# Kernel optimization log

Hardware: AMD Instinct MI355X
Metric: run time of the kernel (lower is better)

The kernel has to match this reference:

```python
import jax, jax.numpy as jnp
import numpy as np

N_NODES = 50000
N_EDGES = 800000
N_GRAPHS = 64
IN_DIM = 128
HID = 32
HEADS = 4
EDGE_DIM = 8
OUT = 10


def setup_inputs() -> dict:
    key = jax.random.key(0)
    ks = jax.random.split(key, 20)
    s = 0.1
    inp = {
        "x": jax.random.normal(ks[0], (N_NODES, IN_DIM), jnp.float32),
        "edge_index": jax.random.randint(ks[1], (2, N_EDGES), 0, N_NODES, jnp.int32),
        "edge_attr": jax.random.normal(ks[2], (N_EDGES, EDGE_DIM), jnp.float32),
        "batch": jnp.sort(jax.random.randint(ks[3], (N_NODES,), 0, N_GRAPHS, jnp.int32)),
        # conv1: heads=4, out=32
        "W1": jax.random.normal(ks[4], (IN_DIM, HEADS * HID), jnp.float32) * s,
        "att_src1": jax.random.normal(ks[5], (HEADS, HID), jnp.float32) * s,
        "att_dst1": jax.random.normal(ks[6], (HEADS, HID), jnp.float32) * s,
        "We1": jax.random.normal(ks[7], (EDGE_DIM, HEADS * HID), jnp.float32) * s,
        "att_e1": jax.random.normal(ks[8], (HEADS, HID), jnp.float32) * s,
        "b1": jnp.zeros((HEADS * HID,), jnp.float32),
        # conv2: heads=1, out=32
        "W2": jax.random.normal(ks[9], (HEADS * HID, HID), jnp.float32) * s,
        "att_src2": jax.random.normal(ks[10], (1, HID), jnp.float32) * s,
        "att_dst2": jax.random.normal(ks[11], (1, HID), jnp.float32) * s,
        "We2": jax.random.normal(ks[12], (EDGE_DIM, HID), jnp.float32) * s,
        "att_e2": jax.random.normal(ks[13], (1, HID), jnp.float32) * s,
        "b2": jnp.zeros((HID,), jnp.float32),
        # MLP head
        "W3": jax.random.normal(ks[14], (HID, HID // 2), jnp.float32) * s,
        "b3": jnp.zeros((HID // 2,), jnp.float32),
        "W4": jax.random.normal(ks[15], (HID // 2, OUT), jnp.float32) * s,
        "b4": jnp.zeros((OUT,), jnp.float32),
    }
    return inp


def _gat_conv(x, src, dst, eattr, W, a_s, a_d, We, a_e, b, H, C, N):
    """PyG GATConv math (self-loops already appended to src/dst/eattr)."""
    h = (x @ W).reshape(-1, H, C)            # [N,H,C]
    e = (eattr @ We).reshape(-1, H, C)       # [E,H,C]
    al_s = jnp.sum(h * a_s, -1)              # [N,H]
    al_d = jnp.sum(h * a_d, -1)              # [N,H]
    alpha = al_s[src] + al_d[dst] + jnp.sum(e * a_e, -1)   # [E,H]
    alpha = jax.nn.leaky_relu(alpha, 0.2)
    # segment softmax over incoming edges of each dst node
    m = jax.ops.segment_max(alpha, dst, num_segments=N)
    ealpha = jnp.exp(alpha - m[dst])
    denom = jax.ops.segment_sum(ealpha, dst, num_segments=N)
    ealpha = ealpha / (denom[dst] + 1e-16)
    msg = h[src] * ealpha[:, :, None]        # [E,H,C]
    out = jax.ops.segment_sum(msg, dst, num_segments=N)  # [N,H,C]
    return out.reshape(N, H * C) + b


def _forward(x, edge_index, edge_attr, batch,
             W1, att_src1, att_dst1, We1, att_e1, b1,
             W2, att_src2, att_dst2, We2, att_e2, b2,
             W3, b3, W4, b4):
    N = x.shape[0]
    src, dst = edge_index[0], edge_index[1]
    # add_self_loops with fill_value='mean': loop attr = mean of incoming edge_attr
    cnt = jax.ops.segment_sum(jnp.ones((src.shape[0],), x.dtype), dst, num_segments=N)
    loop_attr = jax.ops.segment_sum(edge_attr, dst, num_segments=N) / jnp.maximum(cnt, 1.0)[:, None]
    ar = jnp.arange(N, dtype=src.dtype)
    src2 = jnp.concatenate([src, ar])
    dst2 = jnp.concatenate([dst, ar])
    eattr2 = jnp.concatenate([edge_attr, loop_attr], axis=0)

    h = _gat_conv(x, src2, dst2, eattr2, W1, att_src1, att_dst1, We1, att_e1, b1, HEADS, HID, N)
    h = jax.nn.elu(h)
    h = _gat_conv(h, src2, dst2, eattr2, W2, att_src2, att_dst2, We2, att_e2, b2, 1, HID, N)
    h = jax.nn.elu(h)
    # global mean pool per graph
    gsum = jax.ops.segment_sum(h, batch, num_segments=N_GRAPHS)
    gcnt = jax.ops.segment_sum(jnp.ones((N,), h.dtype), batch, num_segments=N_GRAPHS)
    g = gsum / jnp.maximum(gcnt, 1.0)[:, None]
    # MLP head (eval mode: dropout is identity)
    z = jax.nn.relu(g @ W3 + b3)
    return z @ W4 + b4


def reference(x, edge_index, edge_attr, batch,
              W1, att_src1, att_dst1, We1, att_e1, b1,
              W2, att_src2, att_dst2, We2, att_e2, b2,
              W3, b3, W4, b4):
    return _forward(x, edge_index, edge_attr, batch,
                    W1, att_src1, att_dst1, We1, att_e1, b1,
                    W2, att_src2, att_dst2, We2, att_e2, b2,
                    W3, b3, W4, b4)
```

## Files before the change

kernel.cpp:

```cpp
#include <hip/hip_runtime.h>
#include <hip/hip_bf16.h>
#include <math.h>

#define N_NODES 50000
#define N_EDGES 800000
#define N_GRAPHS 64
#define IN_DIM 128
#define HID 32
#define HEADS 4
#define EDGE_DIM 8
#define OUT_DIM 10
#define HC 128
#define NB 196
#define EBLK 3125
#define G1HALF 391

__device__ __forceinline__ float leaky(float x){ return x >= 0.f ? x : 0.2f*x; }
__device__ __forceinline__ float elu_f(float x){ return x > 0.f ? x : __expf(x)-1.f; }

__device__ __forceinline__ float bf2f(unsigned short u){
  union { unsigned int i; float f; } v; v.i = ((unsigned int)u) << 16; return v.f;
}
__device__ __forceinline__ unsigned short f2bf(float f){
  union { float f; unsigned int i; } v; v.f = f;
  unsigned int r = v.i + 0x7FFF + ((v.i >> 16) & 1);
  return (unsigned short)(r >> 16);
}

__device__ __forceinline__ void gemm1_body(int bb, float* xs, float* ws,
    const float* __restrict__ x, const float* __restrict__ W1,
    const float* __restrict__ as1, const float* __restrict__ ad1,
    unsigned short* __restrict__ h1b, float* __restrict__ als1, float* __restrict__ ald1){
  int t = threadIdx.x;
  int cg = t & 15, c8 = cg*8, qb = (t >> 4)*4;
  int base = bb * 64;
  for (int i = t; i < 2048; i += 256){
    int node = base + (i >> 5);
    int col = (i & 31) * 4;
    float4 v = make_float4(0,0,0,0);
    if (node < N_NODES) v = *(const float4*)&x[node*IN_DIM + col];
    *(float4*)&xs[(i>>5)*128 + col] = v;
  }
  float acc[4][8];
  #pragma unroll
  for (int q = 0; q < 4; q++)
    #pragma unroll
    for (int i = 0; i < 8; i++) acc[q][i] = 0.f;

  for (int kb = 0; kb < 128; kb += 64){
    __syncthreads();
    for (int i = t; i < 2048; i += 256)
      *(float4*)&ws[i*4] = *(const float4*)&W1[kb*128 + i*4];
    __syncthreads();
    #pragma unroll 4
    for (int k = 0; k < 64; k++){
      float4 w0 = *(float4*)&ws[k*128 + c8];
      float4 w1 = *(float4*)&ws[k*128 + c8 + 4];
      #pragma unroll
      for (int q = 0; q < 4; q++){
        float xv = xs[(qb + q)*128 + kb + k];
        acc[q][0] = fmaf(xv, w0.x, acc[q][0]);
        acc[q][1] = fmaf(xv, w0.y, acc[q][1]);
        acc[q][2] = fmaf(xv, w0.z, acc[q][2]);
        acc[q][3] = fmaf(xv, w0.w, acc[q][3]);
        acc[q][4] = fmaf(xv, w1.x, acc[q][4]);
        acc[q][5] = fmaf(xv, w1.y, acc[q][5]);
        acc[q][6] = fmaf(xv, w1.z, acc[q][6]);
        acc[q][7] = fmaf(xv, w1.w, acc[q][7]);
      }
    }
  }
  int head = cg >> 2;
  float asv[8], adv[8];
  #pragma unroll
  for (int i = 0; i < 8; i++){ asv[i] = as1[c8 + i]; adv[i] = ad1[c8 + i]; }
  #pragma unroll
  for (int q = 0; q < 4; q++){
    int n = base + qb + q;
    if (n >= N_NODES) continue;
    float sa = 0.f, sd = 0.f;
    #pragma unroll
    for (int i = 0; i < 8; i++){
      sa = fmaf(acc[q][i], asv[i], sa);
      sd = fmaf(acc[q][i], adv[i], sd);
    }
    sa += __shfl_xor(sa, 1); sd += __shfl_xor(sd, 1);
    sa += __shfl_xor(sa, 2); sd += __shfl_xor(sd, 2);
    uint4 pk;
    pk.x = (unsigned int)f2bf(acc[q][0]) | ((unsigned int)f2bf(acc[q][1]) << 16);
    pk.y = (unsigned int)f2bf(acc[q][2]) | ((unsigned int)f2bf(acc[q][3]) << 16);
    pk.z = (unsigned int)f2bf(acc[q][4]) | ((unsigned int)f2bf(acc[q][5]) << 16);
    pk.w = (unsigned int)f2bf(acc[q][6]) | ((unsigned int)f2bf(acc[q][7]) << 16);
    *(uint4*)&h1b[n*HC + c8] = pk;
    if ((cg & 3) == 0){ als1[n*4 + head] = sa; ald1[n*4 + head] = sd; }
  }
}

__global__ __launch_bounds__(256) void k_f1(const int* __restrict__ dst, int* __restrict__ cnt,
    const float* __restrict__ x, const float* __restrict__ W1,
    const float* __restrict__ as1, const float* __restrict__ ad1,
    unsigned short* __restrict__ h1b, float* __restrict__ als1, float* __restrict__ ald1){
  __shared__ float smem[16384];
  int m = blockIdx.x % 9, r = blockIdx.x / 9;
  if (m < 8){
    int e = (r*8 + m)*256 + threadIdx.x;
    if (e < N_EDGES) atomicAdd(&cnt[dst[e]], 1);
    return;
  }
  gemm1_body(r, smem, smem + 8192, x, W1, as1, ad1, h1b, als1, ald1);
}

__global__ __launch_bounds__(256) void k_blocksum(const int* __restrict__ cnt, int* __restrict__ bsum){
  __shared__ int sh[256];
  int n = blockIdx.x*256 + threadIdx.x;
  sh[threadIdx.x] = (n < N_NODES) ? cnt[n] : 0;
  __syncthreads();
  for (int off = 128; off > 0; off >>= 1){
    if (threadIdx.x < off) sh[threadIdx.x] += sh[threadIdx.x + off];
    __syncthreads();
  }
  if (threadIdx.x == 0) bsum[blockIdx.x] = sh[0];
}

__global__ __launch_bounds__(256) void k_scanb(const int* __restrict__ bsum, int* __restrict__ bpre){
  __shared__ int sh[256];
  int t = threadIdx.x;
  int v = (t < NB) ? bsum[t] : 0;
  sh[t] = v; __syncthreads();
  for (int off = 1; off < 256; off <<= 1){
    int u = (t >= off) ? sh[t-off] : 0;
    __syncthreads();
    sh[t] += u;
    __syncthreads();
  }
  if (t < NB) bpre[t] = sh[t] - v;
}

__global__ __launch_bounds__(256) void k_rowptr(const int* __restrict__ cnt, const int* __restrict__ bpre,
    int* __restrict__ rowptr, int* __restrict__ wofs){
  __shared__ int sh[256];
  int t = threadIdx.x; int n = blockIdx.x*256 + t;
  int c = (n < N_NODES) ? cnt[n] : 0;
  sh[t] = c; __syncthreads();
  for (int off = 1; off < 256; off <<= 1){
    int u = (t >= off) ? sh[t-off] : 0;
    __syncthreads();
    sh[t] += u;
    __syncthreads();
  }
  int incl = sh[t];
  if (n < N_NODES){
    int rp = bpre[blockIdx.x] + incl - c;
    rowptr[n] = rp;
    wofs[n] = rp;
  }
  if (n == N_NODES-1) rowptr[N_NODES] = bpre[blockIdx.x] + incl;
}

__global__ __launch_bounds__(256) void k_f2(const int* __restrict__ src, const int* __restrict__ dst,
    const float* __restrict__ eattr,
    const float* __restrict__ We1, const float* __restrict__ ae1w,
    const float* __restrict__ We2, const float* __restrict__ ae2w,
    int* __restrict__ wofs, int4* __restrict__ rec,
    const float* __restrict__ x, const float* __restrict__ W1,
    const float* __restrict__ as1, const float* __restrict__ ad1,
    unsigned short* __restrict__ h1b, float* __restrict__ als1, float* __restrict__ ald1){
  __shared__ float smem[16384];
  int m = blockIdx.x % 9, r = blockIdx.x / 9;
  if (m < 8){
    int t = threadIdx.x;
    if (t < 32){
      int d = t >> 2, h = t & 3;
      float s = 0.f;
      for (int c = 0; c < 32; c++) s = fmaf(We1[d*128 + h*32 + c], ae1w[h*32 + c], s);
      smem[d*4 + h] = s;
    } else if (t < 40){
      int d = t - 32;
      float s = 0.f;
      for (int c = 0; c < 32; c++) s = fmaf(We2[d*32 + c], ae2w[c], s);
      smem[32 + d] = s;
    }
    __syncthreads();
    int e = (r*8 + m)*256 + t;
    if (e >= N_EDGES) return;
    int sv = src[e], d = dst[e];
    float4 x0 = *(const float4*)&eattr[e*8];
    float4 x1 = *(const float4*)&eattr[e*8+4];
    float ea[8] = {x0.x,x0.y,x0.z,x0.w,x1.x,x1.y,x1.z,x1.w};
    float4 rr = make_float4(0,0,0,0);
    float r2 = 0.f;
    #pragma unroll
    for (int dd = 0; dd < 8; dd++){
      rr.x = fmaf(ea[dd], smem[dd*4+0], rr.x);
      rr.y = fmaf(ea[dd], smem[dd*4+1], rr.y);
      rr.z = fmaf(ea[dd], smem[dd*4+2], rr.z);
      rr.w = fmaf(ea[dd], smem[dd*4+3], rr.w);
      r2   = fmaf(ea[dd], smem[32+dd], r2);
    }
    int pos = atomicAdd(&wofs[d], 1);
    int4 rv;
    rv.x = sv;
    rv.y = (int)((unsigned int)f2bf(rr.x) | ((unsigned int)f2bf(rr.y) << 16));
    rv.z = (int)((unsigned int)f2bf(rr.z) | ((unsigned int)f2bf(rr.w) << 16));
    rv.w = __float_as_int(r2);
    rec[pos] = rv;
    return;
  }
  gemm1_body(G1HALF + r, smem, smem + 8192, x, W1, as1, ad1, h1b, als1, ald1);
}

__global__ __launch_bounds__(256) void k_conv1(const int* __restrict__ rowptr, const int4* __restrict__ rec,
    const float* __restrict__ als1, const float* __restrict__ ald1,
    const unsigned short* __restrict__ h1b, const float* __restrict__ b1,
    unsigned short* __restrict__ heb){
  int wv = threadIdx.x >> 6, l = threadIdx.x & 63;
  int n = blockIdx.x*4 + wv;
  if (n >= N_NODES) return;
  int c0 = l*2, h = l >> 4;
  int hs1 = (h & 1) * 16;
  float ad = ald1[n*4 + h];
  float den = 0.f, sum_ae = 0.f;
  float2 acc = make_float2(0.f, 0.f);
  int r0 = rowptr[n], r1 = rowptr[n+1];
  int k = r0;
  for (; k + 2 <= r1; k += 2){
    int4 q0 = rec[k], q1 = rec[k+1];
    unsigned int w0 = (h & 2) ? (unsigned int)q0.z : (unsigned int)q0.y;
    unsigned int w1 = (h & 2) ? (unsigned int)q1.z : (unsigned int)q1.y;
    float ae_0 = bf2f((unsigned short)(w0 >> hs1));
    float ae_1 = bf2f((unsigned short)(w1 >> hs1));
    float as_0 = als1[q0.x*4 + h], as_1 = als1[q1.x*4 + h];
    unsigned int hv0 = *(const unsigned int*)(h1b + q0.x*HC + c0);
    unsigned int hv1 = *(const unsigned int*)(h1b + q1.x*HC + c0);
    float p0 = __expf(leaky(as_0 + ad + ae_0));
    float p1 = __expf(leaky(as_1 + ad + ae_1));
    sum_ae += ae_0 + ae_1;
    den += p0 + p1;
    acc.x = fmaf(p0, bf2f((unsigned short)hv0), acc.x);
    acc.y = fmaf(p0, bf2f((unsigned short)(hv0 >> 16)), acc.y);
    acc.x = fmaf(p1, bf2f((unsigned short)hv1), acc.x);
    acc.y = fmaf(p1, bf2f((unsigned short)(hv1 >> 16)), acc.y);
  }
  if (k < r1){
    int4 q = rec[k];
    unsigned int w = (h & 2) ? (unsigned int)q.z : (unsigned int)q.y;
    float aev = bf2f((unsigned short)(w >> hs1));
    float p = __expf(leaky(als1[q.x*4 + h] + ad + aev));
    unsigned int hv = *(const unsigned int*)(h1b + q.x*HC + c0);
    sum_ae += aev; den += p;
    acc.x = fmaf(p, bf2f((unsigned short)hv), acc.x);
    acc.y = fmaf(p, bf2f((unsigned short)(hv >> 16)), acc.y);
  }
  int cn = r1 - r0; if (cn < 1) cn = 1;
  float ps = __expf(leaky(als1[n*4 + h] + ad + sum_ae / (float)cn));
  unsigned int hs = *(const unsigned int*)(h1b + n*HC + c0);
  den += ps;
  acc.x = fmaf(ps, bf2f((unsigned short)hs), acc.x);
  acc.y = fmaf(ps, bf2f((unsigned short)(hs >> 16)), acc.y);
  float inv = 1.f / (den + 1e-16f);
  float o0 = elu_f(fmaf(acc.x, inv, b1[c0]));
  float o1 = elu_f(fmaf(acc.y, inv, b1[c0+1]));
  *(unsigned int*)(heb + n*HC + c0) =
      (unsigned int)f2bf(o0) | ((unsigned int)f2bf(o1) << 16);
}

__global__ __launch_bounds__(256) void k_gemm2(const unsigned short* __restrict__ heb,
    const float* __restrict__ W2, const float* __restrict__ as2, const float* __restrict__ ad2,
    unsigned short* __restrict__ h2b, float* __restrict__ als2, float* __restrict__ ald2){
  __shared__ float ws[128*32];
  __shared__ float xs[16][128];
  int t = threadIdx.x; int c = t & 31; int j = t >> 5;
  int base = blockIdx.x * 16;
  for (int i = t; i < 1024; i += 256)
    *(float4*)&ws[i*4] = *(const float4*)&W2[i*4];
  {
    int node = base + (t >> 4);
    int col = (t & 15) * 8;
    uint4 v = make_uint4(0,0,0,0);
    if (node < N_NODES) v = *(const uint4*)(heb + node*128 + col);
    float* xp = &xs[t>>4][col];
    xp[0] = bf2f((unsigned short)v.x); xp[1] = bf2f((unsigned short)(v.x>>16));
    xp[2] = bf2f((unsigned short)v.y); xp[3] = bf2f((unsigned short)(v.y>>16));
    xp[4] = bf2f((unsigned short)v.z); xp[5] = bf2f((unsigned short)(v.z>>16));
    xp[6] = bf2f((unsigned short)v.w); xp[7] = bf2f((unsigned short)(v.w>>16));
  }
  __syncthreads();
  float s0 = 0.f, s1 = 0.f;
  #pragma unroll 8
  for (int k = 0; k < 128; k++){
    float w = ws[k*32 + c];
    s0 = fmaf(xs[j*2][k],   w, s0);
    s1 = fmaf(xs[j*2+1][k], w, s1);
  }
  float a2c = as2[c], d2c = ad2[c];
  int n0 = base + j*2, n1 = n0 + 1;
  float sa0 = s0*a2c, sd0 = s0*d2c, sa1 = s1*a2c, sd1 = s1*d2c;
  #pragma unroll
  for (int off = 1; off < 32; off <<= 1){
    sa0 += __shfl_xor(sa0, off); sd0 += __shfl_xor(sd0, off);
    sa1 += __shfl_xor(sa1, off); sd1 += __shfl_xor(sd1, off);
  }
  if (n0 < N_NODES){ h2b[n0*32 + c] = f2bf(s0); if (c == 0){ als2[n0] = sa0; ald2[n0] = sd0; } }
  if (n1 < N_NODES){ h2b[n1*32 + c] = f2bf(s1); if (c == 0){ als2[n1] = sa1; ald2[n1] = sd1; } }
}

__global__ __launch_bounds__(256) void k_conv2(const int* __restrict__ rowptr, const int4* __restrict__ rec,
    const float* __restrict__ als2, const float* __restrict__ ald2,
    const unsigned short* __restrict__ h2b, const float* __restrict__ b2, float* __restrict__ out2){
  int wv = threadIdx.x >> 6, l = threadIdx.x & 63;
  int n = blockIdx.x*4 + wv;
  if (n >= N_NODES) return;
  int half = l >> 5, c = l & 31;
  float ad = ald2[n];
  int r0 = rowptr[n], r1 = rowptr[n+1];
  int h0 = (r1 - r0 + 1) >> 1;
  int ks = half ? r0 + h0 : r0;
  int ke = half ? r1 : r0 + h0;
  float den = 0.f, acc = 0.f, sum_ae = 0.f;
  int k = ks;
  for (; k + 2 <= ke; k += 2){
    int4 q0 = rec[k], q1 = rec[k+1];
    float ae_0 = __int_as_float(q0.w), ae_1 = __int_as_float(q1.w);
    float as_0 = als2[q0.x], as_1 = als2[q1.x];
    float hv0 = bf2f(h2b[q0.x*32 + c]);
    float hv1 = bf2f(h2b[q1.x*32 + c]);
    float p0 = __expf(leaky(as_0 + ad + ae_0));
    float p1 = __expf(leaky(as_1 + ad + ae_1));
    sum_ae += ae_0 + ae_1;
    den += p0 + p1;
    acc = fmaf(p0, hv0, acc);
    acc = fmaf(p1, hv1, acc);
  }
  if (k < ke){
    int4 q = rec[k];
    float aev = __int_as_float(q.w);
    float p = __expf(leaky(als2[q.x] + ad + aev));
    float hv = bf2f(h2b[q.x*32 + c]);
    sum_ae += aev; den += p;
    acc = fmaf(p, hv, acc);
  }
  den += __shfl_xor(den, 32);
  acc += __shfl_xor(acc, 32);
  sum_ae += __shfl_xor(sum_ae, 32);
  int cn = r1 - r0; if (cn < 1) cn = 1;
  float ps = __expf(leaky(als2[n] + ad + sum_ae / (float)cn));
  den += ps;
  acc = fmaf(ps, bf2f(h2b[n*32 + c]), acc);
  float val = acc / (den + 1e-16f) + b2[c];
  if (half == 0) out2[n*32 + c] = elu_f(val);
}

__global__ __launch_bounds__(256) void k_pool(const float* __restrict__ out2, const int* __restrict__ batch,
    float* __restrict__ gpool){
  int g = blockIdx.x;
  int a = 0, b = N_NODES;
  while (a < b){ int mid = (a + b) >> 1; if (batch[mid] < g) a = mid + 1; else b = mid; }
  int lo = a;
  a = lo; b = N_NODES;
  while (a < b){ int mid = (a + b) >> 1; if (batch[mid] < g + 1) a = mid + 1; else b = mid; }
  int hi = a;
  int t = threadIdx.x, c = t & 31, r = t >> 5;
  float s = 0.f;
  for (int n = lo + r; n < hi; n += 8) s += out2[n*32 + c];
  __shared__ float sh[256];
  sh[t] = s; __syncthreads();
  if (r == 0){
    for (int q = 1; q < 8; q++) s += sh[q*32 + c];
    int cg = hi - lo; if (cg < 1) cg = 1;
    gpool[g*32 + c] = s / (float)cg;
  }
}

__global__ __launch_bounds__(1024) void k_mlp(const float* __restrict__ gpool, const float* __restrict__ W3,
    const float* __restrict__ b3, const float* __restrict__ W4, const float* __restrict__ b4,
    float* __restrict__ out){
  __shared__ float z[64*16];
  int t = threadIdx.x;
  {
    int g = t >> 4, jj = t & 15;
    float s = b3[jj];
    #pragma unroll
    for (int c = 0; c < 32; c++) s = fmaf(gpool[g*32 + c], W3[c*16 + jj], s);
    z[t] = fmaxf(s, 0.f);
  }
  __syncthreads();
  if (t < 640){
    int g = t / 10, o = t - g*10;
    float s = b4[o];
    #pragma unroll
    for (int jj = 0; jj < 16; jj++) s = fmaf(z[g*16 + jj], W4[jj*10 + o], s);
    out[t] = s;
  }
}

extern "C" void kernel_launch(void* const* d_in, const int* in_sizes, int n_in,
                              void* d_out, int out_size, void* d_ws, size_t ws_size,
                              hipStream_t stream) {
  (void)in_sizes; (void)n_in; (void)out_size; (void)ws_size;
  const float* x     = (const float*)d_in[0];
  const int*   ei    = (const int*)  d_in[1];
  const float* eattr = (const float*)d_in[2];
  const int*   batch = (const int*)  d_in[3];
  const float* W1    = (const float*)d_in[4];
  const float* as1   = (const float*)d_in[5];
  const float* ad1   = (const float*)d_in[6];
  const float* We1   = (const float*)d_in[7];
  const float* ae1w  = (const float*)d_in[8];
  const float* b1    = (const float*)d_in[9];
  const float* W2    = (const float*)d_in[10];
  const float* as2   = (const float*)d_in[11];
  const float* ad2   = (const float*)d_in[12];
  const float* We2   = (const float*)d_in[13];
  const float* ae2w  = (const float*)d_in[14];
  const float* b2    = (const float*)d_in[15];
  const float* W3    = (const float*)d_in[16];
  const float* b3    = (const float*)d_in[17];
  const float* W4    = (const float*)d_in[18];
  const float* b4    = (const float*)d_in[19];
  float* out = (float*)d_out;
  const int* src  = ei;
  const int* dstp = ei + N_EDGES;

  char* p = (char*)d_ws;
  auto alloc = [&](size_t bytes)->void*{ void* r = (void*)p; p += (bytes + 255) & ~(size_t)255; return r; };
  int*    cnt      = (int*)   alloc(4*N_NODES);
  size_t  zero_bytes = (size_t)(p - (char*)d_ws);
  int*    wofs     = (int*)   alloc(4*N_NODES);
  int*    rowptr   = (int*)   alloc(4*(N_NODES+1));
  int*    bsum     = (int*)   alloc(4*NB);
  int*    bpre     = (int*)   alloc(4*NB);
  int4*   rec      = (int4*)  alloc(16*N_EDGES);
  unsigned short* h1b  = (unsigned short*)alloc(2*N_NODES*HC);
  float*  als1     = (float*) alloc(16*N_NODES);
  float*  ald1     = (float*) alloc(16*N_NODES);
  unsigned short* heb  = (unsigned short*)alloc(2*N_NODES*HC);
  unsigned short* h2b  = (unsigned short*)alloc(2*N_NODES*HID);
  float*  als2     = (float*) alloc(4*N_NODES);
  float*  ald2     = (float*) alloc(4*N_NODES);
  float*  out2     = (float*) alloc(4*N_NODES*HID);
  float*  gpool    = (float*) alloc(4*N_GRAPHS*HID);

  const int FGRID = G1HALF * 9;

  hipMemsetAsync(d_ws, 0, zero_bytes, stream);
  k_f1      <<<FGRID, 256, 0, stream>>>(dstp, cnt, x, W1, as1, ad1, h1b, als1, ald1);
  k_blocksum<<<NB,    256, 0, stream>>>(cnt, bsum);
  k_scanb   <<<1,     256, 0, stream>>>(bsum, bpre);
  k_rowptr  <<<NB,    256, 0, stream>>>(cnt, bpre, rowptr, wofs);
  k_f2      <<<FGRID, 256, 0, stream>>>(src, dstp, eattr, We1, ae1w, We2, ae2w,
                                        wofs, rec, x, W1, as1, ad1, h1b, als1, ald1);
  k_conv1   <<<(N_NODES+3)/4, 256, 0, stream>>>(rowptr, rec, als1, ald1, h1b, b1, heb);
  k_gemm2   <<<(N_NODES+15)/16, 256, 0, stream>>>(heb, W2, as2, ad2, h2b, als2, ald2);
  k_conv2   <<<(N_NODES+3)/4, 256, 0, stream>>>(rowptr, rec, als2, ald2, h2b, b2, out2);
  k_pool    <<<N_GRAPHS, 256, 0, stream>>>(out2, batch, gpool);
  k_mlp     <<<1,    1024, 0, stream>>>(gpool, W3, b3, W4, b4, out);
}
```

Measured before the change: 381.4 us.

## Precompute per-edge attention weights and self-loop terms before aggregation kernels

```diff
diff --git a/kernel.cpp b/kernel.cpp
--- a/kernel.cpp
+++ b/kernel.cpp
@@ -13,7 +13,7 @@
 #define HC 128
 #define NB 196
 #define EBLK 3125
-#define G1HALF 391
+#define G1BLK 782
 
 __device__ __forceinline__ float leaky(float x){ return x >= 0.f ? x : 0.2f*x; }
 __device__ __forceinline__ float elu_f(float x){ return x > 0.f ? x : __expf(x)-1.f; }
@@ -25,6 +25,9 @@
   union { float f; unsigned int i; } v; v.f = f;
   unsigned int r = v.i + 0x7FFF + ((v.i >> 16) & 1);
   return (unsigned short)(r >> 16);
+}
+__device__ __forceinline__ unsigned int pk2(float a, float b){
+  return (unsigned int)f2bf(a) | ((unsigned int)f2bf(b) << 16);
 }
 
 __device__ __forceinline__ void gemm1_body(int bb, float* xs, float* ws,
@@ -39,7 +42,7 @@
     int col = (i & 31) * 4;
     float4 v = make_float4(0,0,0,0);
     if (node < N_NODES) v = *(const float4*)&x[node*IN_DIM + col];
-    *(float4*)&xs[(i>>5)*128 + col] = v;
+    *(float4*)&xs[(i>>5)*132 + col] = v;
   }
   float acc[4][8];
   #pragma unroll
@@ -47,18 +50,21 @@
     #pragma unroll
     for (int i = 0; i < 8; i++) acc[q][i] = 0.f;
 
-  for (int kb = 0; kb < 128; kb += 64){
-    __syncthreads();
-    for (int i = t; i < 2048; i += 256)
-      *(float4*)&ws[i*4] = *(const float4*)&W1[kb*128 + i*4];
+  for (int kb = 0; kb < 128; kb += 32){
+    __syncthreads();
+    for (int i = t; i < 1024; i += 256){
+      int k = i >> 5, col4 = i & 31;
+      int pcg = col4 >> 1, plane = col4 & 1;
+      *(float4*)&ws[plane*2048 + k*64 + pcg*4] = *(const float4*)&W1[(kb+k)*128 + col4*4];
+    }
     __syncthreads();
     #pragma unroll 4
-    for (int k = 0; k < 64; k++){
-      float4 w0 = *(float4*)&ws[k*128 + c8];
-      float4 w1 = *(float4*)&ws[k*128 + c8 + 4];
+    for (int k = 0; k < 32; k++){
+      float4 w0 = *(float4*)&ws[k*64 + cg*4];
+      float4 w1 = *(float4*)&ws[2048 + k*64 + cg*4];
       #pragma unroll
       for (int q = 0; q < 4; q++){
-        float xv = xs[(qb + q)*128 + kb + k];
+        float xv = xs[(qb + q)*132 + kb + k];
         acc[q][0] = fmaf(xv, w0.x, acc[q][0]);
         acc[q][1] = fmaf(xv, w0.y, acc[q][1]);
         acc[q][2] = fmaf(xv, w0.z, acc[q][2]);
@@ -87,10 +93,10 @@
     sa += __shfl_xor(sa, 1); sd += __shfl_xor(sd, 1);
     sa += __shfl_xor(sa, 2); sd += __shfl_xor(sd, 2);
     uint4 pk;
-    pk.x = (unsigned int)f2bf(acc[q][0]) | ((unsigned int)f2bf(acc[q][1]) << 16);
-    pk.y = (unsigned int)f2bf(acc[q][2]) | ((unsigned int)f2bf(acc[q][3]) << 16);
-    pk.z = (unsigned int)f2bf(acc[q][4]) | ((unsigned int)f2bf(acc[q][5]) << 16);
-    pk.w = (unsigned int)f2bf(acc[q][6]) | ((unsigned int)f2bf(acc[q][7]) << 16);
+    pk.x = pk2(acc[q][0], acc[q][1]);
+    pk.y = pk2(acc[q][2], acc[q][3]);
+    pk.z = pk2(acc[q][4], acc[q][5]);
+    pk.w = pk2(acc[q][6], acc[q][7]);
     *(uint4*)&h1b[n*HC + c8] = pk;
     if ((cg & 3) == 0){ als1[n*4 + head] = sa; ald1[n*4 + head] = sd; }
   }
@@ -100,14 +106,14 @@
     const float* __restrict__ x, const float* __restrict__ W1,
     const float* __restrict__ as1, const float* __restrict__ ad1,
     unsigned short* __restrict__ h1b, float* __restrict__ als1, float* __restrict__ ald1){
-  __shared__ float smem[16384];
-  int m = blockIdx.x % 9, r = blockIdx.x / 9;
-  if (m < 8){
-    int e = (r*8 + m)*256 + threadIdx.x;
+  __shared__ float smem[12544];
+  int m = blockIdx.x % 5, r = blockIdx.x / 5;
+  if (m < 4){
+    int e = (r*4 + m)*256 + threadIdx.x;
     if (e < N_EDGES) atomicAdd(&cnt[dst[e]], 1);
     return;
   }
-  gemm1_body(r, smem, smem + 8192, x, W1, as1, ad1, h1b, als1, ald1);
+  gemm1_body(r, smem, smem + 8448, x, W1, as1, ad1, h1b, als1, ald1);
 }
 
 __global__ __launch_bounds__(256) void k_blocksum(const int* __restrict__ cnt, int* __restrict__ bsum){
@@ -157,84 +163,134 @@
   if (n == N_NODES-1) rowptr[N_NODES] = bpre[blockIdx.x] + incl;
 }
 
+__device__ __forceinline__ void v_smem(float* v,
+    const float* __restrict__ We1, const float* __restrict__ ae1w,
+    const float* __restrict__ We2, const float* __restrict__ ae2w){
+  int t = threadIdx.x;
+  if (t < 32){
+    int d = t >> 2, h = t & 3;
+    float s = 0.f;
+    for (int c = 0; c < 32; c++) s = fmaf(We1[d*128 + h*32 + c], ae1w[h*32 + c], s);
+    v[d*4 + h] = s;
+  } else if (t < 40){
+    int d = t - 32;
+    float s = 0.f;
+    for (int c = 0; c < 32; c++) s = fmaf(We2[d*32 + c], ae2w[c], s);
+    v[32 + d] = s;
+  }
+  __syncthreads();
+}
+
 __global__ __launch_bounds__(256) void k_f2(const int* __restrict__ src, const int* __restrict__ dst,
     const float* __restrict__ eattr,
     const float* __restrict__ We1, const float* __restrict__ ae1w,
     const float* __restrict__ We2, const float* __restrict__ ae2w,
-    int* __restrict__ wofs, int4* __restrict__ rec,
-    const float* __restrict__ x, const float* __restrict__ W1,
-    const float* __restrict__ as1, const float* __restrict__ ad1,
-    unsigned short* __restrict__ h1b, float* __restrict__ als1, float* __restrict__ ald1){
-  __shared__ float smem[16384];
-  int m = blockIdx.x % 9, r = blockIdx.x / 9;
-  if (m < 8){
-    int t = threadIdx.x;
-    if (t < 32){
-      int d = t >> 2, h = t & 3;
-      float s = 0.f;
-      for (int c = 0; c < 32; c++) s = fmaf(We1[d*128 + h*32 + c], ae1w[h*32 + c], s);
-      smem[d*4 + h] = s;
-    } else if (t < 40){
-      int d = t - 32;
-      float s = 0.f;
-      for (int c = 0; c < 32; c++) s = fmaf(We2[d*32 + c], ae2w[c], s);
-      smem[32 + d] = s;
-    }
-    __syncthreads();
-    int e = (r*8 + m)*256 + t;
-    if (e >= N_EDGES) return;
-    int sv = src[e], d = dst[e];
-    float4 x0 = *(const float4*)&eattr[e*8];
-    float4 x1 = *(const float4*)&eattr[e*8+4];
-    float ea[8] = {x0.x,x0.y,x0.z,x0.w,x1.x,x1.y,x1.z,x1.w};
-    float4 rr = make_float4(0,0,0,0);
-    float r2 = 0.f;
-    #pragma unroll
-    for (int dd = 0; dd < 8; dd++){
-      rr.x = fmaf(ea[dd], smem[dd*4+0], rr.x);
-      rr.y = fmaf(ea[dd], smem[dd*4+1], rr.y);
-      rr.z = fmaf(ea[dd], smem[dd*4+2], rr.z);
-      rr.w = fmaf(ea[dd], smem[dd*4+3], rr.w);
-      r2   = fmaf(ea[dd], smem[32+dd], r2);
-    }
-    int pos = atomicAdd(&wofs[d], 1);
-    int4 rv;
-    rv.x = sv;
-    rv.y = (int)((unsigned int)f2bf(rr.x) | ((unsigned int)f2bf(rr.y) << 16));
-    rv.z = (int)((unsigned int)f2bf(rr.z) | ((unsigned int)f2bf(rr.w) << 16));
-    rv.w = __float_as_int(r2);
-    rec[pos] = rv;
-    return;
-  }
-  gemm1_body(G1HALF + r, smem, smem + 8192, x, W1, as1, ad1, h1b, als1, ald1);
+    const float* __restrict__ als1, const float* __restrict__ ald1,
+    int* __restrict__ wofs, int4* __restrict__ rec, uint4* __restrict__ rec2){
+  __shared__ float v[40];
+  v_smem(v, We1, ae1w, We2, ae2w);
+  int e = blockIdx.x*256 + threadIdx.x;
+  if (e >= N_EDGES) return;
+  int sv = src[e], d = dst[e];
+  float4 x0 = *(const float4*)&eattr[e*8];
+  float4 x1 = *(const float4*)&eattr[e*8+4];
+  float ea[8] = {x0.x,x0.y,x0.z,x0.w,x1.x,x1.y,x1.z,x1.w};
+  float4 r = make_float4(0,0,0,0);
+  float r2 = 0.f;
+  #pragma unroll
+  for (int dd = 0; dd < 8; dd++){
+    r.x = fmaf(ea[dd], v[dd*4+0], r.x);
+    r.y = fmaf(ea[dd], v[dd*4+1], r.y);
+    r.z = fmaf(ea[dd], v[dd*4+2], r.z);
+    r.w = fmaf(ea[dd], v[dd*4+3], r.w);
+    r2  = fmaf(ea[dd], v[32+dd], r2);
+  }
+  float4 as = *(const float4*)&als1[sv*4];
+  float4 ad = *(const float4*)&ald1[d*4];
+  float p0 = __expf(leaky(as.x + ad.x + r.x));
+  float p1 = __expf(leaky(as.y + ad.y + r.y));
+  float p2 = __expf(leaky(as.z + ad.z + r.z));
+  float p3 = __expf(leaky(as.w + ad.w + r.w));
+  int pos = atomicAdd(&wofs[d], 1);
+  int4 rv;
+  rv.x = sv;
+  rv.y = (int)pk2(p0, p1);
+  rv.z = (int)pk2(p2, p3);
+  rv.w = __float_as_int(r2);
+  rec[pos] = rv;
+  uint4 e2;
+  e2.x = pk2(ea[0], ea[1]); e2.y = pk2(ea[2], ea[3]);
+  e2.z = pk2(ea[4], ea[5]); e2.w = pk2(ea[6], ea[7]);
+  rec2[pos] = e2;
+}
+
+__global__ __launch_bounds__(256) void k_self(const int* __restrict__ rowptr,
+    const uint4* __restrict__ rec2, const float* __restrict__ als1, const float* __restrict__ ald1,
+    const float* __restrict__ We1, const float* __restrict__ ae1w,
+    const float* __restrict__ We2, const float* __restrict__ ae2w,
+    float* __restrict__ pself1, float* __restrict__ mae2){
+  __shared__ float v[40];
+  v_smem(v, We1, ae1w, We2, ae2w);
+  int n = blockIdx.x*256 + threadIdx.x;
+  if (n >= N_NODES) return;
+  int r0 = rowptr[n], r1 = rowptr[n+1];
+  float s[8];
+  #pragma unroll
+  for (int i = 0; i < 8; i++) s[i] = 0.f;
+  for (int k = r0; k < r1; k++){
+    uint4 q = rec2[k];
+    s[0] += bf2f((unsigned short)q.x); s[1] += bf2f((unsigned short)(q.x >> 16));
+    s[2] += bf2f((unsigned short)q.y); s[3] += bf2f((unsigned short)(q.y >> 16));
+    s[4] += bf2f((unsigned short)q.z); s[5] += bf2f((unsigned short)(q.z >> 16));
+    s[6] += bf2f((unsigned short)q.w); s[7] += bf2f((unsigned short)(q.w >> 16));
+  }
+  int cn = r1 - r0; if (cn < 1) cn = 1;
+  float inv = 1.f / (float)cn;
+  float m1[4] = {0.f, 0.f, 0.f, 0.f};
+  float m2 = 0.f;
+  #pragma unroll
+  for (int dd = 0; dd < 8; dd++){
+    float mv = s[dd] * inv;
+    m1[0] = fmaf(mv, v[dd*4+0], m1[0]);
+    m1[1] = fmaf(mv, v[dd*4+1], m1[1]);
+    m1[2] = fmaf(mv, v[dd*4+2], m1[2]);
+    m1[3] = fmaf(mv, v[dd*4+3], m1[3]);
+    m2    = fmaf(mv, v[32+dd], m2);
+  }
+  float4 as = *(const float4*)&als1[n*4];
+  float4 ad = *(const float4*)&ald1[n*4];
+  float4 p;
+  p.x = __expf(leaky(as.x + ad.x + m1[0]));
+  p.y = __expf(leaky(as.y + ad.y + m1[1]));
+  p.z = __expf(leaky(as.z + ad.z + m1[2]));
+  p.w = __expf(leaky(as.w + ad.w + m1[3]));
+  *(float4*)&pself1[n*4] = p;
+  mae2[n] = m2;
 }
 
 __global__ __launch_bounds__(256) void k_conv1(const int* __restrict__ rowptr, const int4* __restrict__ rec,
-    const float* __restrict__ als1, const float* __restrict__ ald1,
-    const unsigned short* __restrict__ h1b, const float* __restrict__ b1,
-    unsigned short* __restrict__ heb){
+    const float* __restrict__ pself1, const unsigned short* __restrict__ h1b,
+    const float* __restrict__ b1, unsigned short* __restrict__ heb){
   int wv = threadIdx.x >> 6, l = threadIdx.x & 63;
   int n = blockIdx.x*4 + wv;
   if (n >= N_NODES) return;
   int c0 = l*2, h = l >> 4;
   int hs1 = (h & 1) * 16;
-  float ad = ald1[n*4 + h];
-  float den = 0.f, sum_ae = 0.f;
-  float2 acc = make_float2(0.f, 0.f);
+  float ps = pself1[n*4 + h];
+  unsigned int hsv = *(const unsigned int*)(h1b + n*HC + c0);
+  float den = ps;
+  float2 acc = make_float2(ps * bf2f((unsigned short)hsv),
+                           ps * bf2f((unsigned short)(hsv >> 16)));
   int r0 = rowptr[n], r1 = rowptr[n+1];
   int k = r0;
   for (; k + 2 <= r1; k += 2){
     int4 q0 = rec[k], q1 = rec[k+1];
     unsigned int w0 = (h & 2) ? (unsigned int)q0.z : (unsigned int)q0.y;
     unsigned int w1 = (h & 2) ? (unsigned int)q1.z : (unsigned int)q1.y;
-    float ae_0 = bf2f((unsigned short)(w0 >> hs1));
-    float ae_1 = bf2f((unsigned short)(w1 >> hs1));
-    float as_0 = als1[q0.x*4 + h], as_1 = als1[q1.x*4 + h];
+    float p0 = bf2f((unsigned short)(w0 >> hs1));
+    float p1 = bf2f((unsigned short)(w1 >> hs1));
     unsigned int hv0 = *(const unsigned int*)(h1b + q0.x*HC + c0);
     unsigned int hv1 = *(const unsigned int*)(h1b + q1.x*HC + c0);
-    float p0 = __expf(leaky(as_0 + ad + ae_0));
-    float p1 = __expf(leaky(as_1 + ad + ae_1));
-    sum_ae += ae_0 + ae_1;
     den += p0 + p1;
     acc.x = fmaf(p0, bf2f((unsigned short)hv0), acc.x);
     acc.y = fmaf(p0, bf2f((unsigned short)(hv0 >> 16)), acc.y);
@@ -244,24 +300,16 @@
   if (k < r1){
     int4 q = rec[k];
     unsigned int w = (h & 2) ? (unsigned int)q.z : (unsigned int)q.y;
-    float aev = bf2f((unsigned short)(w >> hs1));
-    float p = __expf(leaky(als1[q.x*4 + h] + ad + aev));
+    float p = bf2f((unsigned short)(w >> hs1));
     unsigned int hv = *(const unsigned int*)(h1b + q.x*HC + c0);
-    sum_ae += aev; den += p;
+    den += p;
     acc.x = fmaf(p, bf2f((unsigned short)hv), acc.x);
     acc.y = fmaf(p, bf2f((unsigned short)(hv >> 16)), acc.y);
   }
-  int cn = r1 - r0; if (cn < 1) cn = 1;
-  float ps = __expf(leaky(als1[n*4 + h] + ad + sum_ae / (float)cn));
-  unsigned int hs = *(const unsigned int*)(h1b + n*HC + c0);
-  den += ps;
-  acc.x = fmaf(ps, bf2f((unsigned short)hs), acc.x);
-  acc.y = fmaf(ps, bf2f((unsigned short)(hs >> 16)), acc.y);
   float inv = 1.f / (den + 1e-16f);
   float o0 = elu_f(fmaf(acc.x, inv, b1[c0]));
   float o1 = elu_f(fmaf(acc.y, inv, b1[c0+1]));
-  *(unsigned int*)(heb + n*HC + c0) =
-      (unsigned int)f2bf(o0) | ((unsigned int)f2bf(o1) << 16);
+  *(unsigned int*)(heb + n*HC + c0) = pk2(o0, o1);
 }
 
 __global__ __launch_bounds__(256) void k_gemm2(const unsigned short* __restrict__ heb,
@@ -304,48 +352,56 @@
   if (n1 < N_NODES){ h2b[n1*32 + c] = f2bf(s1); if (c == 0){ als2[n1] = sa1; ald2[n1] = sd1; } }
 }
 
-__global__ __launch_bounds__(256) void k_conv2(const int* __restrict__ rowptr, const int4* __restrict__ rec,
-    const float* __restrict__ als2, const float* __restrict__ ald2,
+__global__ __launch_bounds__(256) void k_alpha2(const int* __restrict__ rowptr, const int* __restrict__ rec_i,
+    const float* __restrict__ als2, const float* __restrict__ ald2, const float* __restrict__ mae2,
+    float* __restrict__ p2, float* __restrict__ pself2){
+  int n = blockIdx.x*256 + threadIdx.x;
+  if (n >= N_NODES) return;
+  int r0 = rowptr[n], r1 = rowptr[n+1];
+  float adn = ald2[n];
+  for (int k = r0; k < r1; k++){
+    int sv = rec_i[k*4];
+    float ae = __int_as_float(rec_i[k*4 + 3]);
+    p2[k] = __expf(leaky(als2[sv] + adn + ae));
+  }
+  pself2[n] = __expf(leaky(als2[n] + adn + mae2[n]));
+}
+
+__global__ __launch_bounds__(256) void k_conv2(const int* __restrict__ rowptr, const int* __restrict__ rec_i,
+    const float* __restrict__ p2, const float* __restrict__ pself2,
     const unsigned short* __restrict__ h2b, const float* __restrict__ b2, float* __restrict__ out2){
   int wv = threadIdx.x >> 6, l = threadIdx.x & 63;
   int n = blockIdx.x*4 + wv;
   if (n >= N_NODES) return;
   int half = l >> 5, c = l & 31;
-  float ad = ald2[n];
   int r0 = rowptr[n], r1 = rowptr[n+1];
   int h0 = (r1 - r0 + 1) >> 1;
   int ks = half ? r0 + h0 : r0;
   int ke = half ? r1 : r0 + h0;
-  float den = 0.f, acc = 0.f, sum_ae = 0.f;
+  float den = 0.f, acc = 0.f;
+  if (half == 0){
+    float ps = pself2[n];
+    den = ps;
+    acc = ps * bf2f(h2b[n*32 + c]);
+  }
   int k = ks;
   for (; k + 2 <= ke; k += 2){
-    int4 q0 = rec[k], q1 = rec[k+1];
-    float ae_0 = __int_as_float(q0.w), ae_1 = __int_as_float(q1.w);
-    float as_0 = als2[q0.x], as_1 = als2[q1.x];
-    float hv0 = bf2f(h2b[q0.x*32 + c]);
-    float hv1 = bf2f(h2b[q1.x*32 + c]);
-    float p0 = __expf(leaky(as_0 + ad + ae_0));
-    float p1 = __expf(leaky(as_1 + ad + ae_1));
-    sum_ae += ae_0 + ae_1;
-    den += p0 + p1;
-    acc = fmaf(p0, hv0, acc);
-    acc = fmaf(p1, hv1, acc);
+    float pa = p2[k], pb = p2[k+1];
+    int s0 = rec_i[k*4], s1 = rec_i[(k+1)*4];
+    float hv0 = bf2f(h2b[s0*32 + c]);
+    float hv1 = bf2f(h2b[s1*32 + c]);
+    den += pa + pb;
+    acc = fmaf(pa, hv0, acc);
+    acc = fmaf(pb, hv1, acc);
   }
   if (k < ke){
-    int4 q = rec[k];
-    float aev = __int_as_float(q.w);
-    float p = __expf(leaky(als2[q.x] + ad + aev));
-    float hv = bf2f(h2b[q.x*32 + c]);
-    sum_ae += aev; den += p;
-    acc = fmaf(p, hv, acc);
+    float pa = p2[k];
+    int s0 = rec_i[k*4];
+    den += pa;
+    acc = fmaf(pa, bf2f(h2b[s0*32 + c]), acc);
   }
   den += __shfl_xor(den, 32);
   acc += __shfl_xor(acc, 32);
-  sum_ae += __shfl_xor(sum_ae, 32);
-  int cn = r1 - r0; if (cn < 1) cn = 1;
-  float ps = __expf(leaky(als2[n] + ad + sum_ae / (float)cn));
-  den += ps;
-  acc = fmaf(ps, bf2f(h2b[n*32 + c]), acc);
   float val = acc / (den + 1e-16f) + b2[c];
   if (half == 0) out2[n*32 + c] = elu_f(val);
 }
@@ -430,9 +486,14 @@
   int*    bsum     = (int*)   alloc(4*NB);
   int*    bpre     = (int*)   alloc(4*NB);
   int4*   rec      = (int4*)  alloc(16*N_EDGES);
+  uint4*  rec2     = (uint4*) alloc(16*N_EDGES);
+  float*  p2       = (float*) alloc(4*N_EDGES);
   unsigned short* h1b  = (unsigned short*)alloc(2*N_NODES*HC);
   float*  als1     = (float*) alloc(16*N_NODES);
   float*  ald1     = (float*) alloc(16*N_NODES);
+  float*  pself1   = (float*) alloc(16*N_NODES);
+  float*  mae2     = (float*) alloc(4*N_NODES);
+  float*  pself2   = (float*) alloc(4*N_NODES);
   unsigned short* heb  = (unsigned short*)alloc(2*N_NODES*HC);
   unsigned short* h2b  = (unsigned short*)alloc(2*N_NODES*HID);
   float*  als2     = (float*) alloc(4*N_NODES);
@@ -440,18 +501,19 @@
   float*  out2     = (float*) alloc(4*N_NODES*HID);
   float*  gpool    = (float*) alloc(4*N_GRAPHS*HID);
 
-  const int FGRID = G1HALF * 9;
-
   hipMemsetAsync(d_ws, 0, zero_bytes, stream);
-  k_f1      <<<FGRID, 256, 0, stream>>>(dstp, cnt, x, W1, as1, ad1, h1b, als1, ald1);
-  k_blocksum<<<NB,    256, 0, stream>>>(cnt, bsum);
-  k_scanb   <<<1,     256, 0, stream>>>(bsum, bpre);
-  k_rowptr  <<<NB,    256, 0, stream>>>(cnt, bpre, rowptr, wofs);
-  k_f2      <<<FGRID, 256, 0, stream>>>(src, dstp, eattr, We1, ae1w, We2, ae2w,
-                                        wofs, rec, x, W1, as1, ad1, h1b, als1, ald1);
-  k_conv1   <<<(N_NODES+3)/4, 256, 0, stream>>>(rowptr, rec, als1, ald1, h1b, b1, heb);
+  k_f1      <<<G1BLK*5, 256, 0, stream>>>(dstp, cnt, x, W1, as1, ad1, h1b, als1, ald1);
+  k_blocksum<<<NB,      256, 0, stream>>>(cnt, bsum);
+  k_scanb   <<<1,       256, 0, stream>>>(bsum, bpre);
+  k_rowptr  <<<NB,      256, 0, stream>>>(cnt, bpre, rowptr, wofs);
+  k_f2      <<<EBLK,    256, 0, stream>>>(src, dstp, eattr, We1, ae1w, We2, ae2w,
+                                          als1, ald1, wofs, rec, rec2);
+  k_self    <<<NB,      256, 0, stream>>>(rowptr, rec2, als1, ald1, We1, ae1w, We2, ae2w,
+                                          pself1, mae2);
+  k_conv1   <<<(N_NODES+3)/4, 256, 0, stream>>>(rowptr, rec, pself1, h1b, b1, heb);
   k_gemm2   <<<(N_NODES+15)/16, 256, 0, stream>>>(heb, W2, as2, ad2, h2b, als2, ald2);
-  k_conv2   <<<(N_NODES+3)/4, 256, 0, stream>>>(rowptr, rec, als2, ald2, h2b, b2, out2);
+  k_alpha2  <<<NB,      256, 0, stream>>>(rowptr, (const int*)rec, als2, ald2, mae2, p2, pself2);
+  k_conv2   <<<(N_NODES+3)/4, 256, 0, stream>>>(rowptr, (const int*)rec, p2, pself2, h2b, b2, out2);
   k_pool    <<<N_GRAPHS, 256, 0, stream>>>(out2, batch, gpool);
-  k_mlp     <<<1,    1024, 0, stream>>>(gpool, W3, b3, W4, b4, out);
-}
+  k_mlp     <<<1,      1024, 0, stream>>>(gpool, W3, b3, W4, b4, out);
+}
```

Result: slower. 407.4 us (+6.8%).
